# Kernel optimization log

Measured on AMD Instinct MI355X. Metric: run time of the kernel, lower is better.

## Reference

```python
import jax, jax.numpy as jnp
import numpy as np

B, S, D_MODEL, H, D_KV = 2, 2048, 1024, 16, 64
NUM_BUCKETS, MAX_DIST = 32, 128


def _relative_position_bucket(rel_pos, num_buckets=NUM_BUCKETS, max_distance=MAX_DIST):
    # bidirectional (encoder) bucketing, matching T5Attention._relative_position_bucket
    nb = num_buckets // 2
    buckets = (rel_pos > 0).astype(jnp.int32) * nb
    rel = jnp.abs(rel_pos)
    max_exact = nb // 2
    is_small = rel < max_exact
    rel_f = jnp.maximum(rel.astype(jnp.float32), 1.0)  # guard log(0); masked by is_small anyway
    large = max_exact + (
        jnp.log(rel_f / max_exact) / np.log(max_distance / max_exact) * (nb - max_exact)
    ).astype(jnp.int32)
    large = jnp.minimum(large, nb - 1)
    return buckets + jnp.where(is_small, rel, large)


def setup_inputs() -> dict:
    key = jax.random.key(0)
    ks = jax.random.split(key, 6)
    sc = 1.0 / np.sqrt(D_MODEL)
    return {
        "hidden_states": jax.random.normal(ks[0], (B, S, D_MODEL), jnp.float32),
        "Wq": jax.random.normal(ks[1], (D_MODEL, H * D_KV), jnp.float32) * sc,
        "Wk": jax.random.normal(ks[2], (D_MODEL, H * D_KV), jnp.float32) * sc,
        "Wv": jax.random.normal(ks[3], (D_MODEL, H * D_KV), jnp.float32) * sc,
        "Wo": jax.random.normal(ks[4], (H * D_KV, D_MODEL), jnp.float32) * sc,
        "rel_bias_table": jax.random.normal(ks[5], (NUM_BUCKETS, H), jnp.float32),
    }


def reference(hidden_states, Wq, Wk, Wv, Wo, rel_bias_table):
    b, s, _ = hidden_states.shape
    # projections (T5 uses no bias, scale=1.0 in attention)
    q = (hidden_states @ Wq).reshape(b, s, H, D_KV).transpose(0, 2, 1, 3)  # bhsd
    k = (hidden_states @ Wk).reshape(b, s, H, D_KV).transpose(0, 2, 1, 3)
    v = (hidden_states @ Wv).reshape(b, s, H, D_KV).transpose(0, 2, 1, 3)

    # relative position bias: [1, H, S, S]
    ctx = jnp.arange(s)[:, None]
    mem = jnp.arange(s)[None, :]
    buckets = _relative_position_bucket(mem - ctx)          # [S, S]
    pos_bias = rel_bias_table[buckets]                       # [S, S, H]
    pos_bias = pos_bias.transpose(2, 0, 1)[None]             # [1, H, S, S]

    scores = jnp.einsum("bhqd,bhkd->bhqk", q, k) + pos_bias  # scale = 1.0
    probs = jax.nn.softmax(scores, axis=-1)
    attn = jnp.einsum("bhqk,bhkd->bhqd", probs, v)
    attn = attn.transpose(0, 2, 1, 3).reshape(b, s, H * D_KV)
    return attn @ Wo
```

## Files before the change

kernel.cpp:

```cpp
#include <hip/hip_runtime.h>
#include <hip/hip_fp16.h>

#define S_LEN 2048
#define NH 16
#define DK 64
#define DM 1024
#define NB 2
#define QKV_SZ (NB * NH * S_LEN * DK)

typedef _Float16 half8 __attribute__((ext_vector_type(8)));
typedef _Float16 half4v __attribute__((ext_vector_type(4)));
typedef __fp16 fp16x2 __attribute__((ext_vector_type(2)));
typedef float f32x4 __attribute__((ext_vector_type(4)));

static __device__ __forceinline__ half4v pack4(const f32x4 v) {
  fp16x2 lo = __builtin_amdgcn_cvt_pkrtz(v[0], v[1]);
  fp16x2 hi = __builtin_amdgcn_cvt_pkrtz(v[2], v[3]);
  half4v r;
  ((fp16x2*)&r)[0] = lo;
  ((fp16x2*)&r)[1] = hi;
  return r;
}

#define GLL(gp, lp)                                                              \
  __builtin_amdgcn_global_load_lds(                                              \
      (const __attribute__((address_space(1))) unsigned int*)(gp),               \
      (__attribute__((address_space(3))) unsigned int*)(lp), 16, 0, 0)


__global__ __launch_bounds__(256) void conv_f32_f16(const float* __restrict__ in,
                                                    _Float16* __restrict__ out, int n4) {
  int i = blockIdx.x * 256 + threadIdx.x;
  if (i >= n4) return;
  float4 v = ((const float4*)in)[i];
  half4v o;
  o[0] = (_Float16)v.x; o[1] = (_Float16)v.y; o[2] = (_Float16)v.z; o[3] = (_Float16)v.w;
  ((half4v*)out)[i] = o;
}

__global__ __launch_bounds__(256) void transpose_conv4(
    const float* __restrict__ Wq, const float* __restrict__ Wk,
    const float* __restrict__ Wv, const float* __restrict__ Wo,
    _Float16* __restrict__ Wqkvt, _Float16* __restrict__ Wot) {
  __shared__ float tile[32][33];
  int z = blockIdx.z;
  const float* W = (z == 0) ? Wq : (z == 1) ? Wk : (z == 2) ? Wv : Wo;
  _Float16* Wt = (z < 3) ? (Wqkvt + (size_t)z * 1048576) : Wot;
  float scale = (z == 0) ? 1.44269504f : 1.0f;
  int tx = threadIdx.x, ty = threadIdx.y;
  int nx = blockIdx.x * 32 + tx;
  int ky = blockIdx.y * 32;
#pragma unroll
  for (int i = 0; i < 32; i += 8) tile[ty + i][tx] = W[(size_t)(ky + ty + i) * DM + nx];
  __syncthreads();
  int kx = ky + tx;
  int ny = blockIdx.x * 32;
#pragma unroll
  for (int i = 0; i < 32; i += 8)
    Wt[(size_t)(ny + ty + i) * DM + kx] = (_Float16)(tile[tx][ty + i] * scale);
}

__global__ __launch_bounds__(256) void bias_tab_kernel(const float* __restrict__ table,
                                                       float* __restrict__ tab) {
  int i = blockIdx.x * 256 + threadIdx.x;
  if (i >= NH * 4095) return;
  int h = i / 4095, r = i - h * 4095;
  int rel = r - 2047;
  int bucket = rel > 0 ? 16 : 0;
  int a = rel < 0 ? -rel : rel;
  if (a < 8) {
    bucket += a;
  } else {
    int lg = 31 - __clz(a * a);
    int large = 8 + (lg - 6);
    bucket += (large < 15 ? large : 15);
  }
  tab[i] = table[bucket * NH + h] * 1.44269504f;
}

template <int MODE>
__global__ __launch_bounds__(256) void gemm_f16(const _Float16* __restrict__ A,
                                                const _Float16* __restrict__ Bt,
                                                void* __restrict__ Cout,
                                                int M, int N, int K) {
  __shared__ _Float16 As[128 * 32];
  __shared__ _Float16 Bs[128 * 32];
  const int t = threadIdx.x;
  const int m0 = blockIdx.y * 128, n0 = blockIdx.x * 128;
  const int w = t >> 6, lane = t & 63, l15 = lane & 15, quad = lane >> 4;
  const int wr = (w >> 1) * 64, wc = (w & 1) * 64;
  const int swz = (quad ^ (l15 & 3)) * 8;

  f32x4 acc[4][4];
#pragma unroll
  for (int i = 0; i < 4; i++)
#pragma unroll
    for (int j = 0; j < 4; j++) acc[i][j] = (f32x4){0.f, 0.f, 0.f, 0.f};

  for (int k0 = 0; k0 < K; k0 += 32) {
    __syncthreads();
#pragma unroll
    for (int i = 0; i < 2; i++) {
      int id = t + 256 * i;
      int row = id >> 2, c = id & 3;
      int cg = c ^ (row & 3);
      GLL(A + (size_t)(m0 + row) * K + k0 + cg * 8, (char*)As + id * 16);
      GLL(Bt + (size_t)(n0 + row) * K + k0 + cg * 8, (char*)Bs + id * 16);
    }
    __syncthreads();
    half8 af[4], bf[4];
#pragma unroll
    for (int i = 0; i < 4; i++) af[i] = *(const half8*)(As + (wr + i * 16 + l15) * 32 + swz);
#pragma unroll
    for (int i = 0; i < 4; i++) bf[i] = *(const half8*)(Bs + (wc + i * 16 + l15) * 32 + swz);
#pragma unroll
    for (int i = 0; i < 4; i++)
#pragma unroll
      for (int j = 0; j < 4; j++)
        acc[i][j] = __builtin_amdgcn_mfma_f32_16x16x32_f16(af[i], bf[j], acc[i][j], 0, 0, 0);
  }

#pragma unroll
  for (int i = 0; i < 4; i++)
#pragma unroll
    for (int j = 0; j < 4; j++) {
      int row0 = m0 + wr + i * 16 + quad * 4;
      int col = n0 + wc + j * 16 + l15;
      if (MODE == 1) {
#pragma unroll
        for (int r = 0; r < 4; r++)
          ((float*)Cout)[(size_t)(row0 + r) * N + col] = acc[i][j][r];
      } else {
        int which = col >> 10, rem = col & 1023, hh = rem >> 6, dd = rem & 63;
        int bb = row0 >> 11, ss = row0 & 2047;
        _Float16* base = (_Float16*)Cout;
        if (which == 2) {
          *(half4v*)(base + (size_t)2 * QKV_SZ +
                     ((size_t)((bb * NH + hh) * DK + dd)) * S_LEN + ss) = pack4(acc[i][j]);
        } else {
#pragma unroll
          for (int r = 0; r < 4; r++)
            base[(size_t)which * QKV_SZ +
                 ((size_t)((bb * NH + hh) * S_LEN) + ss + r) * DK + dd] = (_Float16)acc[i][j][r];
        }
      }
    }
}

__global__ __launch_bounds__(256, 4) void attn_kernel(
    const _Float16* __restrict__ Q, const _Float16* __restrict__ K,
    const _Float16* __restrict__ Vt, const float* __restrict__ btab,
    _Float16* __restrict__ attn_out) {
  __shared__ _Float16 Ks[2][4096];
  __shared__ _Float16 Vs[2][4096];
  __shared__ float slab[512];

  const int t = threadIdx.x;
  const int Q0 = blockIdx.x * 64;
  const int h = blockIdx.y, b = blockIdx.z;
  const int w = t >> 6, lane = t & 63, l15 = lane & 15, quad = lane >> 4;
  const int qw0 = Q0 + w * 16;
  const int sw7 = l15 & 7;

  const _Float16* Qb = Q + (size_t)(b * NH + h) * S_LEN * DK;
  const _Float16* Kb = K + (size_t)(b * NH + h) * S_LEN * DK;
  const _Float16* Vb = Vt + (size_t)(b * NH + h) * S_LEN * DK;

  for (int i = t; i < 512; i += 256) slab[i] = btab[h * 4095 + 1791 + i];

  half8 qf[2];
#pragma unroll
  for (int dh = 0; dh < 2; dh++)
    qf[dh] = *(const half8*)(Qb + (size_t)(qw0 + l15) * DK + dh * 32 + quad * 8);

  f32x4 o[4];
#pragma unroll
  for (int dt = 0; dt < 4; dt++) o[dt] = (f32x4){0.f, 0.f, 0.f, 0.f};
  float m_ = -INFINITY, l_ = 0.f;

#define STAGE(bs, kk0)                                                           \
  do {                                                                           \
    _Pragma("unroll")                                                            \
    for (int i_ = 0; i_ < 2; i_++) {                                             \
      int id_ = t + 256 * i_;                                                    \
      int row_ = id_ >> 3, c_ = id_ & 7, cg_ = c_ ^ (row_ & 7);                  \
      GLL(Kb + (size_t)((kk0) + row_) * DK + cg_ * 8, (char*)Ks[bs] + id_ * 16); \
      GLL(Vb + (size_t)row_ * S_LEN + (kk0) + cg_ * 8, (char*)Vs[bs] + id_ * 16);\
    }                                                                            \
  } while (0)

  STAGE(0, 0);
  __syncthreads();

  int cur = 0;
  for (int k0 = 0; k0 < S_LEN; k0 += 64) {
    if (k0 + 64 < S_LEN) STAGE(cur ^ 1, k0 + 64);

    const _Float16* Kc = Ks[cur];
    const _Float16* Vc = Vs[cur];

    const int dk0 = k0 - qw0;
    const bool farneg = (dk0 <= -191);
    const bool farpos = (dk0 >= 143);
    const bool nearc = !(farneg || farpos);
    const float cb = farneg ? slab[128] : slab[384];

    f32x4 st[4];
    if (nearc) {
#pragma unroll
      for (int kt = 0; kt < 4; kt++) {
        int i0 = dk0 + kt * 16 + quad * 4 - l15 + 256;
        f32x4 v;
        v[0] = slab[i0]; v[1] = slab[i0 + 1]; v[2] = slab[i0 + 2]; v[3] = slab[i0 + 3];
        st[kt] = v;
      }
    } else {
#pragma unroll
      for (int kt = 0; kt < 4; kt++) st[kt] = (f32x4){0.f, 0.f, 0.f, 0.f};
    }

    half8 kf[4][2];
#pragma unroll
    for (int kt = 0; kt < 4; kt++)
#pragma unroll
      for (int dh = 0; dh < 2; dh++)
        kf[kt][dh] = *(const half8*)(&Kc[(kt * 16 + l15) * 64 + (((dh << 2) + quad) ^ sw7) * 8]);

#pragma unroll
    for (int kt = 0; kt < 4; kt++)
#pragma unroll
      for (int dh = 0; dh < 2; dh++)
        st[kt] = __builtin_amdgcn_mfma_f32_16x16x32_f16(kf[kt][dh], qf[dh], st[kt], 0, 0, 0);

    float cm = fmaxf(fmaxf(st[0][0], st[0][1]), fmaxf(st[0][2], st[0][3]));
#pragma unroll
    for (int kt = 1; kt < 4; kt++)
      cm = fmaxf(cm, fmaxf(fmaxf(st[kt][0], st[kt][1]), fmaxf(st[kt][2], st[kt][3])));
    cm = fmaxf(cm, __shfl_xor(cm, 16));
    cm = fmaxf(cm, __shfl_xor(cm, 32));
    float mc = nearc ? cm : cm + cb;
    if (__any(mc > m_)) {
      float mnew = fmaxf(m_, mc);
      float alpha = __builtin_amdgcn_exp2f(m_ - mnew);
      m_ = mnew;
      l_ *= alpha;
#pragma unroll
      for (int dt = 0; dt < 4; dt++) o[dt] *= alpha;
    }
    float msub = nearc ? m_ : m_ - cb;

    half4v p16[4];
    f32x4 lacc = (f32x4){0.f, 0.f, 0.f, 0.f};
#pragma unroll
    for (int kt = 0; kt < 4; kt++) {
      f32x4 p;
#pragma unroll
      for (int r = 0; r < 4; r++) p[r] = __builtin_amdgcn_exp2f(st[kt][r] - msub);
      lacc += p;
      p16[kt] = pack4(p);
    }
    l_ += (lacc[0] + lacc[1]) + (lacc[2] + lacc[3]);

#pragma unroll
    for (int dt = 0; dt < 4; dt++) {
      half4v vf[4];
#pragma unroll
      for (int kt = 0; kt < 4; kt++)
        vf[kt] = *(const half4v*)(&Vc[(dt * 16 + l15) * 64 +
                                      ((2 * kt + (quad >> 1)) ^ sw7) * 8 + (quad & 1) * 4]);
#pragma unroll
      for (int kt = 0; kt < 4; kt++)
        o[dt] = __builtin_amdgcn_mfma_f32_16x16x16f16(vf[kt], p16[kt], o[dt], 0, 0, 0);
    }

    __syncthreads();
    cur ^= 1;
  }
#undef STAGE

  float lf = l_;
  lf += __shfl_xor(lf, 16);
  lf += __shfl_xor(lf, 32);
  float inv = 1.0f / lf;
  int q = qw0 + l15;
#pragma unroll
  for (int dt = 0; dt < 4; dt++) {
    f32x4 ov = o[dt] * inv;
    *(half4v*)(attn_out + ((size_t)(b * S_LEN + q)) * DM + h * DK + dt * 16 + quad * 4) =
        pack4(ov);
  }
}

extern "C" void kernel_launch(void* const* d_in, const int* in_sizes, int n_in,
                              void* d_out, int out_size, void* d_ws, size_t ws_size,
                              hipStream_t stream) {
  const float* hs  = (const float*)d_in[0];
  const float* Wq  = (const float*)d_in[1];
  const float* Wk  = (const float*)d_in[2];
  const float* Wv  = (const float*)d_in[3];
  const float* Wo  = (const float*)d_in[4];
  const float* tbl = (const float*)d_in[5];
  float* out = (float*)d_out;
  char* ws = (char*)d_ws;

  _Float16* Xh    = (_Float16*)(ws);
  _Float16* Wqkvt = (_Float16*)(ws + (8u << 20));
  _Float16* Wot   = (_Float16*)(ws + (14u << 20));
  _Float16* Qd    = (_Float16*)(ws + (16u << 20));
  _Float16* Kd    = Qd + (size_t)QKV_SZ;
  _Float16* Vd    = Qd + (size_t)2 * QKV_SZ;
  _Float16* Ah    = (_Float16*)(ws + (40u << 20));
  float*    btab  = (float*)(ws + (48u << 20));

  conv_f32_f16<<<4096, 256, 0, stream>>>(hs, Xh, (NB * S_LEN * DM) / 4);
  transpose_conv4<<<dim3(32, 32, 4), dim3(32, 8), 0, stream>>>(Wq, Wk, Wv, Wo, Wqkvt, Wot);
  bias_tab_kernel<<<256, 256, 0, stream>>>(tbl, btab);

  gemm_f16<0><<<dim3(24, 32), 256, 0, stream>>>(Xh, Wqkvt, (void*)Qd, NB * S_LEN, 3 * DM, DM);
  attn_kernel<<<dim3(S_LEN / 64, NH, NB), 256, 0, stream>>>(Qd, Kd, Vd, btab, Ah);
  gemm_f16<1><<<dim3(8, 32), 256, 0, stream>>>(Ah, Wot, (void*)out, NB * S_LEN, DM, DM);
}
```

Before: 220.3 us.

## Restructure attention inner loop: permuted K layout, MFMA row sums, unrolled double buffer

Reworks the flash-attention inner loop. K rows are stored in a permuted shared-memory order so each lane reads V with wide half8 loads matching a reordered key mapping, and the bias slab indexing follows the same permutation. The softmax denominator is now computed with an MFMA against a ones vector instead of VALU adds plus cross-lane shuffles. The loop is also unrolled by two with fixed buffer indices, staging addresses are precomputed, and s_setprio is raised around MFMA blocks. The aim is to cut LDS instruction count, VALU work and address arithmetic, at the cost of extra MFMA issues and a more fragile index mapping.

```diff
diff --git a/kernel.cpp b/kernel.cpp
--- a/kernel.cpp
+++ b/kernel.cpp
@@ -167,6 +167,27 @@
   const _Float16* Vb = Vt + (size_t)(b * NH + h) * S_LEN * DK;
 
   for (int i = t; i < 512; i += 256) slab[i] = btab[h * 4095 + 1791 + i];
+  const float cbn = btab[h * 4095 + 1791 + 128];
+  const float cbp = btab[h * 4095 + 1791 + 384];
+
+  const int id0 = t, id1 = t + 256;
+  const int r0_ = id0 >> 3, cg0 = (id0 & 7) ^ (r0_ & 7), p0 = r0_ & 31;
+  const int sr0 = (r0_ & 32) | (((p0 >> 2) & 3) << 3) | ((p0 >> 4) << 2) | (p0 & 3);
+  const int r1_ = id1 >> 3, cg1 = (id1 & 7) ^ (r1_ & 7), p1 = r1_ & 31;
+  const int sr1 = (r1_ & 32) | (((p1 >> 2) & 3) << 3) | ((p1 >> 4) << 2) | (p1 & 3);
+  const int kofa = sr0 * DK + cg0 * 8, kofb = sr1 * DK + cg1 * 8;
+  const int vofa = r0_ * S_LEN + cg0 * 8, vofb = r1_ * S_LEN + cg1 * 8;
+  const int lda = id0 * 16, ldb = id1 * 16;
+
+#define STAGE(bs, kk0)                                   \
+  do {                                                   \
+    const _Float16* kp_ = Kb + (size_t)(kk0) * DK;       \
+    const _Float16* vp_ = Vb + (kk0);                    \
+    GLL(kp_ + kofa, (char*)Ks[bs] + lda);                \
+    GLL(kp_ + kofb, (char*)Ks[bs] + ldb);                \
+    GLL(vp_ + vofa, (char*)Vs[bs] + lda);                \
+    GLL(vp_ + vofb, (char*)Vs[bs] + ldb);                \
+  } while (0)
 
   half8 qf[2];
 #pragma unroll
@@ -176,112 +197,101 @@
   f32x4 o[4];
 #pragma unroll
   for (int dt = 0; dt < 4; dt++) o[dt] = (f32x4){0.f, 0.f, 0.f, 0.f};
-  float m_ = -INFINITY, l_ = 0.f;
-
-#define STAGE(bs, kk0)                                                           \
-  do {                                                                           \
-    _Pragma("unroll")                                                            \
-    for (int i_ = 0; i_ < 2; i_++) {                                             \
-      int id_ = t + 256 * i_;                                                    \
-      int row_ = id_ >> 3, c_ = id_ & 7, cg_ = c_ ^ (row_ & 7);                  \
-      GLL(Kb + (size_t)((kk0) + row_) * DK + cg_ * 8, (char*)Ks[bs] + id_ * 16); \
-      GLL(Vb + (size_t)row_ * S_LEN + (kk0) + cg_ * 8, (char*)Vs[bs] + id_ * 16);\
-    }                                                                            \
-  } while (0)
+  f32x4 lac = (f32x4){0.f, 0.f, 0.f, 0.f};
+  float m_ = -INFINITY;
+  const half4v ones = {(_Float16)1.f, (_Float16)1.f, (_Float16)1.f, (_Float16)1.f};
+
+  const int rd0 = l15 * 64 + (quad ^ sw7) * 8;
+  const int rd1 = rd0 ^ 32;
 
   STAGE(0, 0);
   __syncthreads();
 
-  int cur = 0;
-  for (int k0 = 0; k0 < S_LEN; k0 += 64) {
-    if (k0 + 64 < S_LEN) STAGE(cur ^ 1, k0 + 64);
-
-    const _Float16* Kc = Ks[cur];
-    const _Float16* Vc = Vs[cur];
-
-    const int dk0 = k0 - qw0;
-    const bool farneg = (dk0 <= -191);
-    const bool farpos = (dk0 >= 143);
-    const bool nearc = !(farneg || farpos);
-    const float cb = farneg ? slab[128] : slab[384];
-
-    f32x4 st[4];
-    if (nearc) {
-#pragma unroll
-      for (int kt = 0; kt < 4; kt++) {
-        int i0 = dk0 + kt * 16 + quad * 4 - l15 + 256;
-        f32x4 v;
-        v[0] = slab[i0]; v[1] = slab[i0 + 1]; v[2] = slab[i0 + 2]; v[3] = slab[i0 + 3];
-        st[kt] = v;
-      }
-    } else {
-#pragma unroll
-      for (int kt = 0; kt < 4; kt++) st[kt] = (f32x4){0.f, 0.f, 0.f, 0.f};
-    }
-
-    half8 kf[4][2];
-#pragma unroll
-    for (int kt = 0; kt < 4; kt++)
-#pragma unroll
-      for (int dh = 0; dh < 2; dh++)
-        kf[kt][dh] = *(const half8*)(&Kc[(kt * 16 + l15) * 64 + (((dh << 2) + quad) ^ sw7) * 8]);
-
-#pragma unroll
-    for (int kt = 0; kt < 4; kt++)
-#pragma unroll
-      for (int dh = 0; dh < 2; dh++)
-        st[kt] = __builtin_amdgcn_mfma_f32_16x16x32_f16(kf[kt][dh], qf[dh], st[kt], 0, 0, 0);
-
-    float cm = fmaxf(fmaxf(st[0][0], st[0][1]), fmaxf(st[0][2], st[0][3]));
-#pragma unroll
-    for (int kt = 1; kt < 4; kt++)
-      cm = fmaxf(cm, fmaxf(fmaxf(st[kt][0], st[kt][1]), fmaxf(st[kt][2], st[kt][3])));
-    cm = fmaxf(cm, __shfl_xor(cm, 16));
-    cm = fmaxf(cm, __shfl_xor(cm, 32));
-    float mc = nearc ? cm : cm + cb;
-    if (__any(mc > m_)) {
-      float mnew = fmaxf(m_, mc);
-      float alpha = __builtin_amdgcn_exp2f(m_ - mnew);
-      m_ = mnew;
-      l_ *= alpha;
-#pragma unroll
-      for (int dt = 0; dt < 4; dt++) o[dt] *= alpha;
-    }
-    float msub = nearc ? m_ : m_ - cb;
-
-    half4v p16[4];
-    f32x4 lacc = (f32x4){0.f, 0.f, 0.f, 0.f};
-#pragma unroll
-    for (int kt = 0; kt < 4; kt++) {
-      f32x4 p;
-#pragma unroll
-      for (int r = 0; r < 4; r++) p[r] = __builtin_amdgcn_exp2f(st[kt][r] - msub);
-      lacc += p;
-      p16[kt] = pack4(p);
-    }
-    l_ += (lacc[0] + lacc[1]) + (lacc[2] + lacc[3]);
-
-#pragma unroll
-    for (int dt = 0; dt < 4; dt++) {
-      half4v vf[4];
-#pragma unroll
-      for (int kt = 0; kt < 4; kt++)
-        vf[kt] = *(const half4v*)(&Vc[(dt * 16 + l15) * 64 +
-                                      ((2 * kt + (quad >> 1)) ^ sw7) * 8 + (quad & 1) * 4]);
-#pragma unroll
-      for (int kt = 0; kt < 4; kt++)
-        o[dt] = __builtin_amdgcn_mfma_f32_16x16x16f16(vf[kt], p16[kt], o[dt], 0, 0, 0);
-    }
-
-    __syncthreads();
-    cur ^= 1;
+#define TILE(c, kk, stage_ok)                                                         \
+  do {                                                                                \
+    if (stage_ok) STAGE((c) ^ 1, (kk) + 64);   \
+    const int dk0 = (kk) - qw0;                                                       \
+    const bool farneg = (dk0 <= -191);                                                \
+    const bool farpos = (dk0 >= 143);                                                 \
+    const bool nearc = !(farneg || farpos);                                           \
+    const float cb = farneg ? cbn : cbp;                                              \
+    f32x4 st[4];                                                                      \
+    if (nearc) {                                                                      \
+      _Pragma("unroll") for (int kt = 0; kt < 4; kt++) {                              \
+        int i0 = dk0 + (kt >> 1) * 32 + quad * 8 + (kt & 1) * 4 - l15 + 256;          \
+        f32x4 v_;                                                                     \
+        v_[0] = slab[i0]; v_[1] = slab[i0 + 1];                                       \
+        v_[2] = slab[i0 + 2]; v_[3] = slab[i0 + 3];                                   \
+        st[kt] = v_;                                                                  \
+      }                                                                               \
+    } else {                                                                          \
+      _Pragma("unroll") for (int kt = 0; kt < 4; kt++)                                \
+          st[kt] = (f32x4){0.f, 0.f, 0.f, 0.f};                                       \
+    }                                                                                 \
+    half8 kf0[4], kf1[4];                                                             \
+    _Pragma("unroll") for (int kt = 0; kt < 4; kt++) {                                \
+      kf0[kt] = *(const half8*)(&Ks[c][rd0 + kt * 1024]);                             \
+      kf1[kt] = *(const half8*)(&Ks[c][rd1 + kt * 1024]);                             \
+    }                                                                                 \
+    __builtin_amdgcn_s_setprio(1);                                                    \
+    _Pragma("unroll") for (int kt = 0; kt < 4; kt++) {                                \
+      st[kt] = __builtin_amdgcn_mfma_f32_16x16x32_f16(kf0[kt], qf[0], st[kt], 0, 0, 0); \
+      st[kt] = __builtin_amdgcn_mfma_f32_16x16x32_f16(kf1[kt], qf[1], st[kt], 0, 0, 0); \
+    }                                                                                 \
+    __builtin_amdgcn_s_setprio(0);                                                    \
+                                                         \
+    float x0 = fmaxf(fmaxf(st[0][0], st[0][1]), st[0][2]);                            \
+    float x1 = fmaxf(fmaxf(st[0][3], st[1][0]), st[1][1]);                            \
+    float x2 = fmaxf(fmaxf(st[1][2], st[1][3]), st[2][0]);                            \
+    float x3 = fmaxf(fmaxf(st[2][1], st[2][2]), st[2][3]);                            \
+    float x4 = fmaxf(fmaxf(st[3][0], st[3][1]), st[3][2]);                            \
+    float cm = fmaxf(fmaxf(fmaxf(x0, x1), fmaxf(x2, x3)), fmaxf(x4, st[3][3]));       \
+    cm = fmaxf(cm, __shfl_xor(cm, 16));                                               \
+    cm = fmaxf(cm, __shfl_xor(cm, 32));                                               \
+    float mc = nearc ? cm : cm + cb;                                                  \
+    if (__any(mc > m_)) {           \
+      float mnew = fmaxf(m_, mc);                                                     \
+      float alpha = __builtin_amdgcn_exp2f(m_ - mnew);                                \
+      m_ = mnew;                                                                      \
+      lac *= alpha;                                                                   \
+      _Pragma("unroll") for (int dt = 0; dt < 4; dt++) o[dt] *= alpha;                \
+    }                                                                                 \
+    float msub = nearc ? m_ : m_ - cb;                                                \
+    half4v p16[4];                                                                    \
+    _Pragma("unroll") for (int kt = 0; kt < 4; kt++) {                                \
+      f32x4 p_;                                                                       \
+      _Pragma("unroll") for (int r = 0; r < 4; r++)                                   \
+          p_[r] = __builtin_amdgcn_exp2f(st[kt][r] - msub);                           \
+      p16[kt] = pack4(p_);                                                            \
+    }                                                                                 \
+    __builtin_amdgcn_s_setprio(1);                                                    \
+     \
+    _Pragma("unroll") for (int kt = 0; kt < 4; kt++)                                  \
+        lac = __builtin_amdgcn_mfma_f32_16x16x16f16(ones, p16[kt], lac, 0, 0, 0);     \
+    _Pragma("unroll") for (int dt = 0; dt < 4; dt++) {                                \
+      half8 va_ = *(const half8*)(&Vs[c][rd0 + dt * 1024]);                           \
+      half8 vb_ = *(const half8*)(&Vs[c][rd1 + dt * 1024]);                           \
+      half4v alo = {va_[0], va_[1], va_[2], va_[3]};                                  \
+      half4v ahi = {va_[4], va_[5], va_[6], va_[7]};                                  \
+      half4v blo = {vb_[0], vb_[1], vb_[2], vb_[3]};                                  \
+      half4v bhi = {vb_[4], vb_[5], vb_[6], vb_[7]};                                  \
+      o[dt] = __builtin_amdgcn_mfma_f32_16x16x16f16(alo, p16[0], o[dt], 0, 0, 0);     \
+      o[dt] = __builtin_amdgcn_mfma_f32_16x16x16f16(ahi, p16[1], o[dt], 0, 0, 0);     \
+      o[dt] = __builtin_amdgcn_mfma_f32_16x16x16f16(blo, p16[2], o[dt], 0, 0, 0);     \
+      o[dt] = __builtin_amdgcn_mfma_f32_16x16x16f16(bhi, p16[3], o[dt], 0, 0, 0);     \
+    }                                                                                 \
+    __builtin_amdgcn_s_setprio(0);                                                    \
+    __syncthreads();              \
+  } while (0)
+
+  for (int k0 = 0; k0 < S_LEN; k0 += 128) {
+    TILE(0, k0, 1);
+    TILE(1, k0 + 64, (k0 + 128 < S_LEN));
   }
+#undef TILE
 #undef STAGE
 
-  float lf = l_;
-  lf += __shfl_xor(lf, 16);
-  lf += __shfl_xor(lf, 32);
-  float inv = 1.0f / lf;
+  float inv = 1.0f / lac[0];
   int q = qw0 + l15;
 #pragma unroll
   for (int dt = 0; dt < 4; dt++) {
```

New measurement: 215.7 us. -2.1%, faster.
